# Kernel optimization log

Measured on AMD Instinct MI355X. Metric: run time of the kernel, lower is better.

Reference implementation:

```python
import jax, jax.numpy as jnp
import numpy as np

TYPE_NUM = 40000
REL_NUM = 10000
N = TYPE_NUM + REL_NUM  # 50000 nodes
E = 800000              # edges (avg degree 16)
EMB, MID, OUT = 256, 256, 128


def setup_inputs() -> dict:
    key = jax.random.key(0)
    k0, k1, k2, k3 = jax.random.split(key, 4)
    # xavier-ish scales
    node_emb = jax.random.normal(k0, (N, EMB), jnp.float32) * (1.0 / np.sqrt(EMB))
    W1 = jax.random.normal(k1, (EMB, MID), jnp.float32) * (1.0 / np.sqrt(EMB))
    W2 = jax.random.normal(k2, (MID, OUT), jnp.float32) * (1.0 / np.sqrt(MID))
    b1 = jnp.zeros((MID,), jnp.float32)
    b2 = jnp.zeros((OUT,), jnp.float32)
    edge_index = jax.random.randint(k3, (2, E), 0, N, jnp.int32)
    return {"node_emb": node_emb, "W1": W1, "b1": b1, "W2": W2, "b2": b2,
            "edge_index": edge_index}


def _gcn_conv(X, W, b, src, dst):
    """torch_geometric GCNConv: x' = D^-1/2 (A+I) D^-1/2 (X W) + b."""
    n = X.shape[0]
    loop = jnp.arange(n, dtype=src.dtype)
    s = jnp.concatenate([src, loop])  # source j
    d = jnp.concatenate([dst, loop])  # target i
    deg = jax.ops.segment_sum(jnp.ones_like(d, dtype=X.dtype), d, num_segments=n)
    dis = jnp.where(deg > 0, jax.lax.rsqrt(deg), 0.0)
    h = X @ W                               # [n, out]
    norm = (dis[s] * dis[d])[:, None]       # [E+n, 1]
    msg = h[s] * norm                       # gather messages
    return jax.ops.segment_sum(msg, d, num_segments=n) + b


def reference(node_emb, W1, b1, W2, b2, edge_index):
    src, dst = edge_index[0], edge_index[1]
    # torch nn.GELU default is exact (erf) gelu
    X = jax.nn.gelu(_gcn_conv(node_emb, W1, b1, src, dst), approximate=False)
    X = jax.nn.gelu(_gcn_conv(X, W2, b2, src, dst), approximate=False)
    return X[:TYPE_NUM], X[TYPE_NUM:]
```

## Files before the change

### kernel.cpp

```cpp
#include <hip/hip_runtime.h>
#include <math.h>

#define EMB 256
#define MID 256
#define OUTF 128
#define KDIM 256
#define LDK 40
#define SLOT 64

using frag_ab = __attribute__((ext_vector_type(8))) short;
using frag_cd = __attribute__((ext_vector_type(4))) float;
typedef float f32x2 __attribute__((ext_vector_type(2)));

__device__ __forceinline__ float gelu_exact(float x) {
    return 0.5f * x * (1.0f + erff(x * 0.70710678118654752f));
}

__device__ __forceinline__ unsigned short f2bf(float f) {
    union { float f; unsigned int i; } v;
    v.f = f;
    unsigned int r = v.i + 0x7fff + ((v.i >> 16) & 1);
    return (unsigned short)(r >> 16);
}

__device__ __forceinline__ f32x2 bfpair(unsigned int u) {
    union { unsigned int i; float f; } a, b;
    a.i = u << 16;
    b.i = u & 0xffff0000u;
    f32x2 r;
    r.x = a.f; r.y = b.f;
    return r;
}


__global__ __launch_bounds__(256) void init_kernel(
    const float* __restrict__ W1, const float* __restrict__ W2,
    unsigned short* __restrict__ W1t, unsigned short* __restrict__ W2t,
    int* __restrict__ cnt, unsigned short* __restrict__ h1pad,
    unsigned short* __restrict__ h2pad, int n, int zb) {
    int b = blockIdx.x;
    int tid = threadIdx.x;
    if (b < zb) {
        int i = b * 256 + tid;
        if (i < n) cnt[i] = 0;
        return;
    }
    b -= zb;
    if (b < 256) {
        int id = b * 256 + tid;
        int k = id >> 8, nn = id & 255;
        W1t[(size_t)nn * EMB + k] = f2bf(W1[(size_t)k * MID + nn]);
        return;
    }
    b -= 256;
    if (b < 128) {
        int id = b * 256 + tid;
        int k = id >> 7, nn = id & 127;
        W2t[(size_t)nn * MID + k] = f2bf(W2[(size_t)k * OUTF + nn]);
        return;
    }
    h1pad[tid] = 0;
    if (tid < OUTF) h2pad[tid] = 0;
}


__global__ void rank_scatter(const int* __restrict__ src, const int* __restrict__ dst,
                             int* __restrict__ cnt, int* __restrict__ slots, int E) {
    int e = blockIdx.x * blockDim.x + threadIdx.x;
    if (e < E) {
        int d = dst[e];
        int r = atomicAdd(&cnt[d], 1);
        if (r < SLOT) slots[(size_t)d * SLOT + r] = src[e];
    }
}


template <bool A_FP32, int NT>
__global__ __launch_bounds__(256, 2) void mfma_gemm(const void* __restrict__ Av,
                                                    const unsigned short* __restrict__ Wt,
                                                    const int* __restrict__ cnt,
                                                    unsigned short* __restrict__ C,
                                                    int M) {
    constexpr int Ntot = NT * 128;
    __shared__ __align__(16) unsigned short As[128 * LDK];
    __shared__ __align__(16) unsigned short Bs[NT * 128 * LDK];

    const int tid = threadIdx.x;
    const int m0 = blockIdx.x * 128;
    const int wave = tid >> 6, lane = tid & 63;
    const int wrow = (wave >> 1) * 64, wcol = (wave & 1) * 64;
    const int q = lane >> 4, r = lane & 15;

    frag_cd acc[NT][4][4] = {};

    const int qb = tid & 3;
    const int nb = tid >> 2;

    for (int ks = 0; ks < KDIM; ks += 32) {
        if (A_FP32) {
            const float* A = (const float*)Av;
            int qa = tid & 7;
            int ra = tid >> 3;
#pragma unroll
            for (int rr = 0; rr < 4; ++rr) {
                int row = ra + rr * 32;
                int grow = m0 + row;
                if (grow >= M) grow = M - 1;
                float4 v = *(const float4*)(A + (size_t)grow * KDIM + ks + qa * 4);
                ushort4 w;
                w.x = f2bf(v.x); w.y = f2bf(v.y); w.z = f2bf(v.z); w.w = f2bf(v.w);
                *(ushort4*)&As[row * LDK + qa * 4] = w;
            }
        } else {
            const unsigned short* A = (const unsigned short*)Av;
#pragma unroll
            for (int rr = 0; rr < 2; ++rr) {
                int row = nb + rr * 64;
                int grow = m0 + row;
                if (grow >= M) grow = M - 1;
                uint4 v = *(const uint4*)(A + (size_t)grow * KDIM + ks + qb * 8);
                *(uint4*)&As[row * LDK + qb * 8] = v;
            }
        }
#pragma unroll
        for (int rr = 0; rr < 2 * NT; ++rr) {
            int n = nb + rr * 64;
            uint4 v = *(const uint4*)(Wt + (size_t)n * KDIM + ks + qb * 8);
            *(uint4*)&Bs[n * LDK + qb * 8] = v;
        }
        __syncthreads();

        frag_ab af[4];
#pragma unroll
        for (int i = 0; i < 4; ++i)
            af[i] = *(const frag_ab*)&As[(wrow + i * 16 + r) * LDK + q * 8];
#pragma unroll
        for (int nt = 0; nt < NT; ++nt) {
            frag_ab bfr[4];
#pragma unroll
            for (int j = 0; j < 4; ++j)
                bfr[j] = *(const frag_ab*)&Bs[(nt * 128 + wcol + j * 16 + r) * LDK + q * 8];
#pragma unroll
            for (int i = 0; i < 4; ++i)
#pragma unroll
                for (int j = 0; j < 4; ++j)
                    acc[nt][i][j] = __builtin_amdgcn_mfma_f32_16x16x32_bf16(
                        af[i], bfr[j], acc[nt][i][j], 0, 0, 0);
        }
        __syncthreads();
    }

#pragma unroll
    for (int i = 0; i < 4; ++i)
#pragma unroll
        for (int g = 0; g < 4; ++g) {
            int row = m0 + wrow + i * 16 + q * 4 + g;
            if (row < M) {
                float sc = rsqrtf((float)(cnt[row] + 1));
#pragma unroll
                for (int nt = 0; nt < NT; ++nt)
#pragma unroll
                    for (int j = 0; j < 4; ++j) {
                        int col = nt * 128 + wcol + j * 16 + r;
                        C[(size_t)row * Ntot + col] = f2bf(acc[nt][i][j][g] * sc);
                    }
            }
        }
}


template <int VEC> struct ldt;
template <> struct ldt<4> { using T = uint2; };
template <> struct ldt<2> { using T = unsigned int; };

template <int F, bool OUT_BF>
__global__ __launch_bounds__(256) void agg_gelu4(const unsigned short* __restrict__ h,
                                                 const int* __restrict__ cnt,
                                                 const int* __restrict__ slots,
                                                 const float* __restrict__ bias,
                                                 void* __restrict__ out, int n) {
    constexpr int VEC = F / 64;
    using LT = typename ldt<VEC>::T;
    int wid = (blockIdx.x * 256 + threadIdx.x) >> 6;
    int lane = threadIdx.x & 63;
    if (wid >= n) return;
    const int c0 = lane * VEC;
    const unsigned short* hb = h + c0;

    int deg = cnt[wid];
    float di = rsqrtf((float)(deg + 1));
    int m = deg < SLOT ? deg : SLOT;

    f32x2 acc[VEC / 2];
    {
        LT s = *(const LT*)(hb + (size_t)wid * F);
        const unsigned int* u = (const unsigned int*)&s;
#pragma unroll
        for (int p = 0; p < VEC / 2; ++p) acc[p] = bfpair(u[p]);
    }

    if (m > 0) {
        int jmine = (lane < m) ? slots[(size_t)wid * SLOT + lane] : n;
        int mp = (m + 7) & ~7;

        LT A[8], B[8];
        auto load8 = [&](LT* buf, int t) {
#pragma unroll
            for (int u = 0; u < 8; ++u) {
                int j = __builtin_amdgcn_readlane(jmine, t + u);
                buf[u] = *(const LT*)(hb + (size_t)j * F);
            }
        };
        auto acc8 = [&](const LT* buf) {
#pragma unroll
            for (int u = 0; u < 8; ++u) {
                const unsigned int* w = (const unsigned int*)&buf[u];
#pragma unroll
                for (int p = 0; p < VEC / 2; ++p) acc[p] += bfpair(w[p]);
            }
        };

        load8(A, 0);
        int t = 8;
        for (;;) {
            if (t >= mp) { acc8(A); break; }
            load8(B, t); acc8(A); t += 8;
            if (t >= mp) { acc8(B); break; }
            load8(A, t); acc8(B); t += 8;
        }
    }

    float res[VEC];
#pragma unroll
    for (int p = 0; p < VEC / 2; ++p) {
        res[2 * p + 0] = gelu_exact(di * acc[p].x + bias[c0 + 2 * p + 0]);
        res[2 * p + 1] = gelu_exact(di * acc[p].y + bias[c0 + 2 * p + 1]);
    }

    if (OUT_BF) {
        unsigned short* ob = (unsigned short*)out + (size_t)wid * F + c0;
        if (VEC == 4) {
            uint2 pk;
            pk.x = (unsigned int)f2bf(res[0]) | ((unsigned int)f2bf(res[1]) << 16);
            pk.y = (unsigned int)f2bf(res[2]) | ((unsigned int)f2bf(res[3]) << 16);
            *(uint2*)ob = pk;
        } else {
            unsigned int pk = (unsigned int)f2bf(res[0]) | ((unsigned int)f2bf(res[1]) << 16);
            *(unsigned int*)ob = pk;
        }
    } else {
        float* ob = (float*)out + (size_t)wid * F + c0;
        if (VEC == 4) {
            float4 rv; rv.x = res[0]; rv.y = res[1]; rv.z = res[2]; rv.w = res[3];
            *(float4*)ob = rv;
        } else {
            float2 rv; rv.x = res[0]; rv.y = res[1];
            *(float2*)ob = rv;
        }
    }
}


extern "C" void kernel_launch(void* const* d_in, const int* in_sizes, int n_in,
                              void* d_out, int out_size, void* d_ws, size_t ws_size,
                              hipStream_t stream) {
    const float* node_emb = (const float*)d_in[0];
    const float* W1 = (const float*)d_in[1];
    const float* b1 = (const float*)d_in[2];
    const float* W2 = (const float*)d_in[3];
    const float* b2 = (const float*)d_in[4];
    const int* edge_index = (const int*)d_in[5];

    const int N = in_sizes[0] / EMB;
    const int E = in_sizes[5] / 2;
    const int* src = edge_index;
    const int* dst = edge_index + E;

    char* ws = (char*)d_ws;
    size_t off = 0;
    auto alloc = [&](size_t bytes) -> void* {
        off = (off + 255) & ~(size_t)255;
        void* p = ws + off;
        off += bytes;
        return p;
    };

    const int nb = (N + 255) / 256;

    int* cnt = (int*)alloc((size_t)N * 4);
    int* slots = (int*)alloc((size_t)N * SLOT * 4);
    unsigned short* W1t = (unsigned short*)alloc((size_t)EMB * MID * 2);
    unsigned short* W2t = (unsigned short*)alloc((size_t)MID * OUTF * 2);
    unsigned short* h1 = (unsigned short*)alloc((size_t)(N + 1) * MID * 2);
    unsigned short* h2 = (unsigned short*)alloc((size_t)(N + 1) * OUTF * 2);
    unsigned short* X1 = (unsigned short*)alloc((size_t)N * MID * 2);

    init_kernel<<<nb + 256 + 128 + 1, 256, 0, stream>>>(
        W1, W2, W1t, W2t, cnt, h1 + (size_t)N * MID, h2 + (size_t)N * OUTF, N, nb);
    rank_scatter<<<(E + 255) / 256, 256, 0, stream>>>(src, dst, cnt, slots, E);
    mfma_gemm<true, 2><<<(N + 127) / 128, 256, 0, stream>>>(node_emb, W1t, cnt, h1, N);
    agg_gelu4<256, true><<<(N + 3) / 4, 256, 0, stream>>>(h1, cnt, slots, b1, X1, N);
    mfma_gemm<false, 1><<<(N + 127) / 128, 256, 0, stream>>>(X1, W2t, cnt, h2, N);
    agg_gelu4<128, false><<<(N + 3) / 4, 256, 0, stream>>>(h2, cnt, slots, b2, d_out, N);
}
```

Before: 259.6 us.

## Store hidden features in column-sliced layout for cache-local gathers

Stores the GEMM outputs h1/h2 and the intermediate X1 as 8 column slices (node-major within each slice). The aggregation kernel is rewritten so each block handles one slice for a group of nodes, with several nodes per wave and neighbor indices spread across lanes and shuffled. The goal is a per-slice gather working set small enough to stay in L2/MALL, so random neighbor reads hit cache more often. In exchange, each gather is narrower (64B or 32B rows), the slot list and degree are re-read once per slice, and the GEMM writes become strided scatters.

```diff
diff --git a/kernel.cpp b/kernel.cpp
--- a/kernel.cpp
+++ b/kernel.cpp
@@ -36,8 +36,8 @@
 __global__ __launch_bounds__(256) void init_kernel(
     const float* __restrict__ W1, const float* __restrict__ W2,
     unsigned short* __restrict__ W1t, unsigned short* __restrict__ W2t,
-    int* __restrict__ cnt, unsigned short* __restrict__ h1pad,
-    unsigned short* __restrict__ h2pad, int n, int zb) {
+    int* __restrict__ cnt, unsigned short* __restrict__ h1s,
+    unsigned short* __restrict__ h2s, int n, int zb) {
     int b = blockIdx.x;
     int tid = threadIdx.x;
     if (b < zb) {
@@ -59,8 +59,14 @@
         W2t[(size_t)nn * MID + k] = f2bf(W2[(size_t)k * OUTF + nn]);
         return;
     }
-    h1pad[tid] = 0;
-    if (tid < OUTF) h2pad[tid] = 0;
+    {
+        int c = tid >> 5, w = tid & 31;
+        h1s[((size_t)c * (n + 1) + n) * 32 + w] = 0;
+    }
+    if (tid < 128) {
+        int c = tid >> 4, w = tid & 15;
+        h2s[((size_t)c * (n + 1) + n) * 16 + w] = 0;
+    }
 }
 
 
@@ -75,13 +81,12 @@
 }
 
 
-template <bool A_FP32, int NT>
+template <bool A_FP32, int NT, int OUT_SC>
 __global__ __launch_bounds__(256, 2) void mfma_gemm(const void* __restrict__ Av,
                                                     const unsigned short* __restrict__ Wt,
                                                     const int* __restrict__ cnt,
                                                     unsigned short* __restrict__ C,
                                                     int M) {
-    constexpr int Ntot = NT * 128;
     __shared__ __align__(16) unsigned short As[128 * LDK];
     __shared__ __align__(16) unsigned short Bs[NT * 128 * LDK];
 
@@ -113,12 +118,13 @@
             }
         } else {
             const unsigned short* A = (const unsigned short*)Av;
+            int cA = ks >> 5;
 #pragma unroll
             for (int rr = 0; rr < 2; ++rr) {
                 int row = nb + rr * 64;
                 int grow = m0 + row;
                 if (grow >= M) grow = M - 1;
-                uint4 v = *(const uint4*)(A + (size_t)grow * KDIM + ks + qb * 8);
+                uint4 v = *(const uint4*)(A + ((size_t)cA * M + grow) * 32 + qb * 8);
                 *(uint4*)&As[row * LDK + qb * 8] = v;
             }
         }
@@ -162,101 +168,79 @@
 #pragma unroll
                     for (int j = 0; j < 4; ++j) {
                         int col = nt * 128 + wcol + j * 16 + r;
-                        C[(size_t)row * Ntot + col] = f2bf(acc[nt][i][j][g] * sc);
+                        int cs = col / OUT_SC, w = col % OUT_SC;
+                        C[((size_t)cs * (M + 1) + row) * OUT_SC + w] =
+                            f2bf(acc[nt][i][j][g] * sc);
                     }
             }
         }
 }
 
 
-template <int VEC> struct ldt;
-template <> struct ldt<4> { using T = uint2; };
-template <> struct ldt<2> { using T = unsigned int; };
-
-template <int F, bool OUT_BF>
-__global__ __launch_bounds__(256) void agg_gelu4(const unsigned short* __restrict__ h,
+template <int COLS, bool OUT_BF>
+__global__ __launch_bounds__(256) void agg_slice(const unsigned short* __restrict__ hs,
                                                  const int* __restrict__ cnt,
                                                  const int* __restrict__ slots,
                                                  const float* __restrict__ bias,
                                                  void* __restrict__ out, int n) {
-    constexpr int VEC = F / 64;
-    using LT = typename ldt<VEC>::T;
-    int wid = (blockIdx.x * 256 + threadIdx.x) >> 6;
-    int lane = threadIdx.x & 63;
-    if (wid >= n) return;
-    const int c0 = lane * VEC;
-    const unsigned short* hb = h + c0;
-
-    int deg = cnt[wid];
+    constexpr int LG = COLS / 4;
+    constexpr int NPW = 64 / LG;
+    const int c = blockIdx.x & 7;
+    const int ib = blockIdx.x >> 3;
+    const int tid = threadIdx.x;
+    const int wave = tid >> 6, lane = tid & 63;
+    const int g = lane / LG, li = lane & (LG - 1);
+    const int node = ib * (4 * NPW) + wave * NPW + g;
+    const bool act = node < n;
+    const int nodeC = act ? node : 0;
+
+    const unsigned short* hc = hs + ((size_t)c * (n + 1)) * COLS + li * 4;
+    const int deg = cnt[nodeC];
+    const int m = act ? (deg < SLOT ? deg : SLOT) : 0;
+    const int* sl = slots + (size_t)nodeC * SLOT;
+
+    f32x2 acc[2];
+    {
+        uint2 s = *(const uint2*)(hc + (size_t)nodeC * COLS);
+        acc[0] = bfpair(s.x);
+        acc[1] = bfpair(s.y);
+    }
+
+    for (int b = 0;; ++b) {
+        int pos = b * LG + li;
+        if (!__ballot(pos < m)) break;
+        int jm = (pos < m) ? sl[pos] : n;
+        uint2 rr[LG];
+#pragma unroll
+        for (int t = 0; t < LG; ++t) {
+            int j = __shfl(jm, (lane & ~(LG - 1)) + t);
+            rr[t] = *(const uint2*)(hc + (size_t)j * COLS);
+        }
+#pragma unroll
+        for (int t = 0; t < LG; ++t) {
+            acc[0] += bfpair(rr[t].x);
+            acc[1] += bfpair(rr[t].y);
+        }
+    }
+
+    if (!act) return;
     float di = rsqrtf((float)(deg + 1));
-    int m = deg < SLOT ? deg : SLOT;
-
-    f32x2 acc[VEC / 2];
-    {
-        LT s = *(const LT*)(hb + (size_t)wid * F);
-        const unsigned int* u = (const unsigned int*)&s;
-#pragma unroll
-        for (int p = 0; p < VEC / 2; ++p) acc[p] = bfpair(u[p]);
-    }
-
-    if (m > 0) {
-        int jmine = (lane < m) ? slots[(size_t)wid * SLOT + lane] : n;
-        int mp = (m + 7) & ~7;
-
-        LT A[8], B[8];
-        auto load8 = [&](LT* buf, int t) {
-#pragma unroll
-            for (int u = 0; u < 8; ++u) {
-                int j = __builtin_amdgcn_readlane(jmine, t + u);
-                buf[u] = *(const LT*)(hb + (size_t)j * F);
-            }
-        };
-        auto acc8 = [&](const LT* buf) {
-#pragma unroll
-            for (int u = 0; u < 8; ++u) {
-                const unsigned int* w = (const unsigned int*)&buf[u];
-#pragma unroll
-                for (int p = 0; p < VEC / 2; ++p) acc[p] += bfpair(w[p]);
-            }
-        };
-
-        load8(A, 0);
-        int t = 8;
-        for (;;) {
-            if (t >= mp) { acc8(A); break; }
-            load8(B, t); acc8(A); t += 8;
-            if (t >= mp) { acc8(B); break; }
-            load8(A, t); acc8(B); t += 8;
-        }
-    }
-
-    float res[VEC];
-#pragma unroll
-    for (int p = 0; p < VEC / 2; ++p) {
-        res[2 * p + 0] = gelu_exact(di * acc[p].x + bias[c0 + 2 * p + 0]);
-        res[2 * p + 1] = gelu_exact(di * acc[p].y + bias[c0 + 2 * p + 1]);
-    }
+    const float* bb = bias + c * COLS + li * 4;
+    float res[4];
+    res[0] = gelu_exact(di * acc[0].x + bb[0]);
+    res[1] = gelu_exact(di * acc[0].y + bb[1]);
+    res[2] = gelu_exact(di * acc[1].x + bb[2]);
+    res[3] = gelu_exact(di * acc[1].y + bb[3]);
 
     if (OUT_BF) {
-        unsigned short* ob = (unsigned short*)out + (size_t)wid * F + c0;
-        if (VEC == 4) {
-            uint2 pk;
-            pk.x = (unsigned int)f2bf(res[0]) | ((unsigned int)f2bf(res[1]) << 16);
-            pk.y = (unsigned int)f2bf(res[2]) | ((unsigned int)f2bf(res[3]) << 16);
-            *(uint2*)ob = pk;
-        } else {
-            unsigned int pk = (unsigned int)f2bf(res[0]) | ((unsigned int)f2bf(res[1]) << 16);
-            *(unsigned int*)ob = pk;
-        }
+        uint2 pk;
+        pk.x = (unsigned int)f2bf(res[0]) | ((unsigned int)f2bf(res[1]) << 16);
+        pk.y = (unsigned int)f2bf(res[2]) | ((unsigned int)f2bf(res[3]) << 16);
+        *(uint2*)((unsigned short*)out + ((size_t)c * n + node) * COLS + li * 4) = pk;
     } else {
-        float* ob = (float*)out + (size_t)wid * F + c0;
-        if (VEC == 4) {
-            float4 rv; rv.x = res[0]; rv.y = res[1]; rv.z = res[2]; rv.w = res[3];
-            *(float4*)ob = rv;
-        } else {
-            float2 rv; rv.x = res[0]; rv.y = res[1];
-            *(float2*)ob = rv;
-        }
+        float4 rv;
+        rv.x = res[0]; rv.y = res[1]; rv.z = res[2]; rv.w = res[3];
+        *(float4*)((float*)out + (size_t)node * 128 + c * 16 + li * 4) = rv;
     }
 }
 
@@ -291,15 +275,18 @@
     int* slots = (int*)alloc((size_t)N * SLOT * 4);
     unsigned short* W1t = (unsigned short*)alloc((size_t)EMB * MID * 2);
     unsigned short* W2t = (unsigned short*)alloc((size_t)MID * OUTF * 2);
-    unsigned short* h1 = (unsigned short*)alloc((size_t)(N + 1) * MID * 2);
-    unsigned short* h2 = (unsigned short*)alloc((size_t)(N + 1) * OUTF * 2);
-    unsigned short* X1 = (unsigned short*)alloc((size_t)N * MID * 2);
+    unsigned short* h1s = (unsigned short*)alloc((size_t)8 * (N + 1) * 32 * 2);
+    unsigned short* h2s = (unsigned short*)alloc((size_t)8 * (N + 1) * 16 * 2);
+    unsigned short* X1s = (unsigned short*)alloc((size_t)8 * N * 32 * 2);
 
     init_kernel<<<nb + 256 + 128 + 1, 256, 0, stream>>>(
-        W1, W2, W1t, W2t, cnt, h1 + (size_t)N * MID, h2 + (size_t)N * OUTF, N, nb);
+        W1, W2, W1t, W2t, cnt, h1s, h2s, N, nb);
     rank_scatter<<<(E + 255) / 256, 256, 0, stream>>>(src, dst, cnt, slots, E);
-    mfma_gemm<true, 2><<<(N + 127) / 128, 256, 0, stream>>>(node_emb, W1t, cnt, h1, N);
-    agg_gelu4<256, true><<<(N + 3) / 4, 256, 0, stream>>>(h1, cnt, slots, b1, X1, N);
-    mfma_gemm<false, 1><<<(N + 127) / 128, 256, 0, stream>>>(X1, W2t, cnt, h2, N);
-    agg_gelu4<128, false><<<(N + 3) / 4, 256, 0, stream>>>(h2, cnt, slots, b2, d_out, N);
-}
+    mfma_gemm<true, 2, 32><<<(N + 127) / 128, 256, 0, stream>>>(node_emb, W1t, cnt,
+                                                                h1s, N);
+    agg_slice<32, true><<<((N + 31) / 32) * 8, 256, 0, stream>>>(h1s, cnt, slots, b1,
+                                                                 X1s, N);
+    mfma_gemm<false, 1, 16><<<(N + 127) / 128, 256, 0, stream>>>(X1s, W2t, cnt, h2s, N);
+    agg_slice<16, false><<<((N + 63) / 64) * 8, 256, 0, stream>>>(h2s, cnt, slots, b2,
+                                                                  d_out, N);
+}
```

Measured after the change: 269.0 us. +3.6%, slower.
